# Kernel optimization log

Measured on AMD Instinct MI355X. Metric: run time of the kernel, lower is better.

Reference implementation:

```python
import jax, jax.numpy as jnp
import numpy as np

NEG_SLOPE = 0.2
LN_EPS = 1e-5
NUM_LAYERS = 4
H = 3            # num heads (both modalities)
C_MOL = 512      # molecule channels (in == out, required by the cat in forward)
C_PROT = 1280    # protein channels
VOCAB = 512 * 9 + 1
G_MOL = 512      # molecule graphs
G_PROT = 32      # protein graphs


def _with_self_loops(src, dst, n):
    loop = jnp.arange(n, dtype=src.dtype)
    return jnp.concatenate([src, loop]), jnp.concatenate([dst, loop])


def gat_conv(x, src, dst, W, a_src, a_dst, bias):
    """PyG GATConv, concat=False (head-mean), add_self_loops=True.
    x: [N, Fin], W: [Fin, H*C], a_src/a_dst: [H, C], bias: [C]."""
    n = x.shape[0]
    h = (x @ W).reshape(n, a_src.shape[0], a_src.shape[1])   # [N,H,C]
    al_s = jnp.sum(h * a_src, axis=-1)                       # [N,H]
    al_d = jnp.sum(h * a_dst, axis=-1)                       # [N,H]
    s, d = _with_self_loops(src, dst, n)
    e = jax.nn.leaky_relu(al_s[s] + al_d[d], NEG_SLOPE)      # [E+N,H]
    m = jax.ops.segment_max(e, d, num_segments=n)            # segment softmax (stable)
    m = jnp.where(jnp.isfinite(m), m, 0.0)
    p = jnp.exp(e - m[d])
    z = jax.ops.segment_sum(p, d, num_segments=n)
    alpha = p / (z[d] + 1e-16)                               # [E+N,H]
    out = jax.ops.segment_sum(h[s] * alpha[:, :, None], d, num_segments=n)  # [N,H,C]
    return out.mean(axis=1) + bias                           # concat=False -> head mean


def layer_norm(x, g, b):
    mu = x.mean(-1, keepdims=True)
    var = ((x - mu) ** 2).mean(-1, keepdims=True)
    return (x - mu) * jax.lax.rsqrt(var + LN_EPS) * g + b


def mean_pool(x, batch, num_graphs):
    s = jax.ops.segment_sum(x, batch, num_segments=num_graphs)
    cnt = jax.ops.segment_sum(jnp.ones((x.shape[0],), x.dtype), batch, num_segments=num_graphs)
    return s / jnp.maximum(cnt, 1.0)[:, None]


def setup_inputs() -> dict:
    key = jax.random.key(0)
    ks = jax.random.split(key, 20)
    n_mol, e_mol = 40000, 80000
    n_prot, e_prot = 8000, 64000
    drug_x = jax.random.randint(ks[0], (n_mol, 9), 0, VOCAB)
    mol_edge_index = jax.random.randint(ks[1], (2, e_mol), 0, n_mol)
    mol_batch = jnp.sort(jax.random.randint(ks[2], (n_mol,), 0, G_MOL))
    prot_x = jax.random.normal(ks[3], (n_prot, C_PROT), jnp.float32)
    prot_edge_index = jax.random.randint(ks[4], (2, e_prot), 0, n_prot)
    prot_batch = jnp.sort(jax.random.randint(ks[5], (n_prot,), 0, G_PROT))
    sc = 0.02
    emb = (jax.random.normal(ks[6], (VOCAB, C_MOL), jnp.float32) * sc).at[0].set(0.0)  # padding_idx=0
    mol_W = jax.random.normal(ks[7], (NUM_LAYERS, C_MOL, H * C_MOL), jnp.float32) * sc
    mol_asrc = jax.random.normal(ks[8], (NUM_LAYERS, H, C_MOL), jnp.float32) * sc
    mol_adst = jax.random.normal(ks[9], (NUM_LAYERS, H, C_MOL), jnp.float32) * sc
    mol_bias = jnp.zeros((NUM_LAYERS, C_MOL), jnp.float32)
    mol_ln_g = jnp.ones((NUM_LAYERS, C_MOL), jnp.float32)
    mol_ln_b = jnp.zeros((NUM_LAYERS, C_MOL), jnp.float32)
    prot_W = jax.random.normal(ks[10], (NUM_LAYERS, C_PROT, H * C_PROT), jnp.float32) * sc
    prot_asrc = jax.random.normal(ks[11], (NUM_LAYERS, H, C_PROT), jnp.float32) * sc
    prot_adst = jax.random.normal(ks[12], (NUM_LAYERS, H, C_PROT), jnp.float32) * sc
    prot_bias = jnp.zeros((NUM_LAYERS, C_PROT), jnp.float32)
    prot_ln_g = jnp.ones((NUM_LAYERS, C_PROT), jnp.float32)
    prot_ln_b = jnp.zeros((NUM_LAYERS, C_PROT), jnp.float32)
    return dict(drug_x=drug_x, mol_edge_index=mol_edge_index, mol_batch=mol_batch,
                prot_x=prot_x, prot_edge_index=prot_edge_index, prot_batch=prot_batch,
                emb=emb, mol_W=mol_W, mol_asrc=mol_asrc, mol_adst=mol_adst,
                mol_bias=mol_bias, mol_ln_g=mol_ln_g, mol_ln_b=mol_ln_b,
                prot_W=prot_W, prot_asrc=prot_asrc, prot_adst=prot_adst,
                prot_bias=prot_bias, prot_ln_g=prot_ln_g, prot_ln_b=prot_ln_b)


def reference(drug_x, mol_edge_index, mol_batch, prot_x, prot_edge_index, prot_batch,
              emb, mol_W, mol_asrc, mol_adst, mol_bias, mol_ln_g, mol_ln_b,
              prot_W, prot_asrc, prot_adst, prot_bias, prot_ln_g, prot_ln_b):
    # dropout layers are identity (eval mode)
    mol_x = emb[drug_x].mean(axis=-2)                       # [N_mol, C_MOL]
    mol_feats = [mean_pool(mol_x, mol_batch, G_MOL)]
    prot_feats = [mean_pool(prot_x, prot_batch, G_PROT)]
    msrc, mdst = mol_edge_index[0], mol_edge_index[1]
    psrc, pdst = prot_edge_index[0], prot_edge_index[1]
    px = prot_x
    for i in range(NUM_LAYERS):
        mol_x = gat_conv(mol_x, msrc, mdst, mol_W[i], mol_asrc[i], mol_adst[i], mol_bias[i])
        mol_x = layer_norm(mol_x, mol_ln_g[i], mol_ln_b[i])
        px = gat_conv(px, psrc, pdst, prot_W[i], prot_asrc[i], prot_adst[i], prot_bias[i])
        px = layer_norm(px, prot_ln_g[i], prot_ln_b[i])
        mol_feats.append(mean_pool(mol_x, mol_batch, G_MOL))
        prot_feats.append(mean_pool(px, prot_batch, G_PROT))
    return jnp.stack(mol_feats, axis=1), jnp.stack(prot_feats, axis=1)  # [G,5,C] each
```

## Files before the change

kernel.cpp:

```cpp
#include <hip/hip_runtime.h>
#include <cstdint>


constexpr int H_HEADS = 3;
constexpr float NEG_SLOPE = 0.2f;
constexpr float LN_EPS = 1e-5f;
constexpr int N_MOL = 40000, E_MOL = 80000, C_MOL = 512, G_MOL = 512;
constexpr int N_PROT = 8000, E_PROT = 64000, C_PROT = 1280, G_PROT = 32;
constexpr int LAYERS = 4;
constexpr int MPAD_MOL = 40064;
constexpr int MPAD_PROT = 8064;

typedef unsigned short u16;
typedef __attribute__((ext_vector_type(8))) short short8v;
typedef __attribute__((ext_vector_type(4))) unsigned short ushort4v;
typedef __attribute__((ext_vector_type(4))) float f32x4;

__device__ __forceinline__ float bf2f(u16 s) {
    union { unsigned u; float f; } v; v.u = ((unsigned)s) << 16; return v.f;
}
__device__ __forceinline__ u16 f2bf(float f) {
    union { float f; unsigned u; } v; v.f = f;
    return (u16)((v.u + 0x7fffu + ((v.u >> 16) & 1u)) >> 16);
}

__device__ __forceinline__ void g2l16(const void* g, void* l) {
    __builtin_amdgcn_global_load_lds((const __attribute__((address_space(1))) void*)g,
                                     (__attribute__((address_space(3))) void*)l, 16, 0, 0);
}


__global__ void set_int_kernel(int* p, int v, int n) {
    int i = blockIdx.x * blockDim.x + threadIdx.x;
    if (i < n) p[i] = v;
}

__global__ void zero_f32_kernel(float* p, int n) {
    int i = blockIdx.x * blockDim.x + threadIdx.x;
    if (i < n) p[i] = 0.f;
}

__global__ void copy_int_kernel(const int* __restrict__ s, int* __restrict__ d, int n) {
    int i = blockIdx.x * blockDim.x + threadIdx.x;
    if (i < n) d[i] = s[i];
}

__global__ void hist_kernel(const int* __restrict__ keys, int n, int* __restrict__ cnt) {
    int i = blockIdx.x * blockDim.x + threadIdx.x;
    if (i < n) atomicAdd(&cnt[keys[i]], 1);
}

__global__ void scan_kernel(const int* __restrict__ in, int* __restrict__ out, int n) {
    __shared__ int sums[1024];
    const int t = threadIdx.x;
    const int chunk = (n + 1023) / 1024;
    const int start = t * chunk;
    const int end = min(start + chunk, n);
    int s = 0;
    for (int i = start; i < end; ++i) s += in[i];
    sums[t] = s;
    __syncthreads();
    if (t == 0) {
        int acc = 0;
        for (int i = 0; i < 1024; ++i) { int v = sums[i]; sums[i] = acc; acc += v; }
        out[n] = acc;
    }
    __syncthreads();
    int acc = sums[t];
    for (int i = start; i < end; ++i) { out[i] = acc; acc += in[i]; }
}

__global__ void fill_self_kernel(int* __restrict__ pos, int* __restrict__ srcl, int n) {
    int i = blockIdx.x * blockDim.x + threadIdx.x;
    if (i < n) { int slot = atomicAdd(&pos[i], 1); srcl[slot] = i; }
}

__global__ void fill_edge_kernel(const int* __restrict__ src, const int* __restrict__ dst, int e,
                                 int* __restrict__ pos, int* __restrict__ srcl) {
    int i = blockIdx.x * blockDim.x + threadIdx.x;
    if (i < e) { int slot = atomicAdd(&pos[dst[i]], 1); srcl[slot] = src[i]; }
}

__global__ void f32_to_bf16(const float* __restrict__ in, u16* __restrict__ out, int n) {
    int i = blockIdx.x * blockDim.x + threadIdx.x;
    if (i < n) out[i] = f2bf(in[i]);
}


__global__ void embed_mean_kernel(const int* __restrict__ drug_x, const float* __restrict__ emb,
                                  u16* __restrict__ out) {
    const int n = blockIdx.x;
    __shared__ int idx[9];
    if (threadIdx.x < 9) idx[threadIdx.x] = drug_x[n * 9 + threadIdx.x];
    __syncthreads();
    const int c = threadIdx.x;
    float s = 0.f;
#pragma unroll
    for (int t = 0; t < 9; ++t) s += emb[(size_t)idx[t] * C_MOL + c];
    out[(size_t)n * C_MOL + c] = f2bf(s * (1.f / 9.f));
}


__global__ __launch_bounds__(256) void transfold(const float* __restrict__ W, u16* __restrict__ Wt,
                                                 const float* __restrict__ asrc,
                                                 const float* __restrict__ adst,
                                                 float* __restrict__ wsrc, float* __restrict__ wdst,
                                                 int CIN, int COUT, size_t headStride, int ldn) {
    __shared__ float t[32][33];
    __shared__ float rs[8][33], rd[8][33];
    const int h = blockIdx.z;
    const int n0 = blockIdx.x * 32, k0 = blockIdx.y * 32;
    const int tx = threadIdx.x & 31, ty = threadIdx.x >> 5;
#pragma unroll
    for (int q = 0; q < 4; ++q)
        t[ty + q * 8][tx] = W[(size_t)(k0 + ty + q * 8) * (H_HEADS * COUT) + h * COUT + n0 + tx];
    __syncthreads();
#pragma unroll
    for (int q = 0; q < 4; ++q)
        Wt[(size_t)h * headStride + (size_t)(n0 + ty + q * 8) * ldn + k0 + tx] =
            f2bf(t[tx][ty + q * 8]);
    float ps = 0.f, pd = 0.f;
    const float* as = asrc + h * COUT + n0;
    const float* ad = adst + h * COUT + n0;
#pragma unroll
    for (int q = 0; q < 4; ++q) {
        const float w = t[tx][ty + q * 8];
        ps += w * as[ty + q * 8];
        pd += w * ad[ty + q * 8];
    }
    rs[ty][tx] = ps;
    rd[ty][tx] = pd;
    __syncthreads();
    if (ty == 0) {
        float s = 0.f, d = 0.f;
#pragma unroll
        for (int j = 0; j < 8; ++j) { s += rs[j][tx]; d += rd[j][tx]; }
        atomicAdd(&wsrc[h * CIN + k0 + tx], s);
        atomicAdd(&wdst[h * CIN + k0 + tx], d);
    }
}


template <int C>
__global__ void attn_logits(const u16* __restrict__ x, const float* __restrict__ wsrc,
                            const float* __restrict__ wdst, float* __restrict__ als,
                            float* __restrict__ ald) {
    constexpr int PER = C / 64;
    const int n = blockIdx.x, lane = threadIdx.x;
    const u16* xr = x + (size_t)n * C + lane * PER;
    float xv[PER];
#pragma unroll
    for (int i = 0; i < PER; i += 4) {
        const ushort4v v = *(const ushort4v*)(xr + i);
        xv[i] = bf2f(v.x); xv[i + 1] = bf2f(v.y); xv[i + 2] = bf2f(v.z); xv[i + 3] = bf2f(v.w);
    }
    for (int h = 0; h < H_HEADS; ++h) {
        const float* ws = wsrc + h * C + lane * PER;
        const float* wd = wdst + h * C + lane * PER;
        float ss = 0.f, sd = 0.f;
#pragma unroll
        for (int i = 0; i < PER; i += 4) {
            const float4 a = *(const float4*)(ws + i);
            const float4 b = *(const float4*)(wd + i);
            ss += xv[i] * a.x + xv[i + 1] * a.y + xv[i + 2] * a.z + xv[i + 3] * a.w;
            sd += xv[i] * b.x + xv[i + 1] * b.y + xv[i + 2] * b.z + xv[i + 3] * b.w;
        }
        for (int o = 32; o; o >>= 1) { ss += __shfl_down(ss, o); sd += __shfl_down(sd, o); }
        if (lane == 0) { als[n * H_HEADS + h] = ss; ald[n * H_HEADS + h] = sd; }
    }
}


__global__ void alpha_kernel2(const float* __restrict__ als, const float* __restrict__ ald,
                              const int* __restrict__ indptr, const int* __restrict__ srcl,
                              float* __restrict__ alphaw, int n_nodes) {
    const int t = blockIdx.x * blockDim.x + threadIdx.x;
    const int n = t / H_HEADS, h = t - n * H_HEADS;
    if (n >= n_nodes) return;
    const int beg = indptr[n], end = indptr[n + 1];
    const float ad = ald[n * H_HEADS + h];
    float m = -1e30f;
    for (int e = beg; e < end; ++e) {
        float v = als[srcl[e] * H_HEADS + h] + ad;
        v = v >= 0.f ? v : NEG_SLOPE * v;
        m = fmaxf(m, v);
    }
    float z = 0.f;
    for (int e = beg; e < end; ++e) {
        float v = als[srcl[e] * H_HEADS + h] + ad;
        v = v >= 0.f ? v : NEG_SLOPE * v;
        z += __expf(v - m);
    }
    const float zi = 1.f / (z + 1e-16f);
    for (int e = beg; e < end; ++e) {
        float v = als[srcl[e] * H_HEADS + h] + ad;
        v = v >= 0.f ? v : NEG_SLOPE * v;
        alphaw[e * H_HEADS + h] = __expf(v - m) * zi;
    }
}


__global__ __launch_bounds__(256) void aggregate_mol(const u16* __restrict__ x,
                                                     const float* __restrict__ alphaw,
                                                     const int* __restrict__ indptr,
                                                     const int* __restrict__ srcl,
                                                     u16* __restrict__ agg) {
    const int wv = threadIdx.x >> 6, lane = threadIdx.x & 63;
    const int n = blockIdx.x * 4 + wv;
    const int beg = indptr[n], end = indptr[n + 1];
    float acc[H_HEADS][8];
#pragma unroll
    for (int h = 0; h < H_HEADS; ++h)
#pragma unroll
        for (int j = 0; j < 8; ++j) acc[h][j] = 0.f;
    for (int e = beg; e < end; ++e) {
        const float a0 = alphaw[e * H_HEADS + 0];
        const float a1 = alphaw[e * H_HEADS + 1];
        const float a2 = alphaw[e * H_HEADS + 2];
        const short8v row = *(const short8v*)(x + (size_t)srcl[e] * C_MOL + lane * 8);
#pragma unroll
        for (int j = 0; j < 8; ++j) {
            const float f = bf2f((u16)row[j]);
            acc[0][j] += a0 * f; acc[1][j] += a1 * f; acc[2][j] += a2 * f;
        }
    }
    u16* o = agg + (size_t)n * (3 * C_MOL) + lane * 8;
#pragma unroll
    for (int h = 0; h < H_HEADS; ++h) {
        short8v r;
#pragma unroll
        for (int j = 0; j < 8; ++j) r[j] = (short)f2bf(acc[h][j]);
        *(short8v*)(o + h * C_MOL) = r;
    }
}


template <int C>
__global__ void aggregate_all3(const u16* __restrict__ x, const float* __restrict__ alphaw,
                               const int* __restrict__ indptr, const int* __restrict__ srcl,
                               u16* __restrict__ agg) {
    const int n = blockIdx.x, tid = threadIdx.x;
    const int beg = indptr[n], end = indptr[n + 1];
    float acc[H_HEADS][4];
#pragma unroll
    for (int h = 0; h < H_HEADS; ++h)
#pragma unroll
        for (int j = 0; j < 4; ++j) acc[h][j] = 0.f;
    for (int e = beg; e < end; ++e) {
        const float a0 = alphaw[e * H_HEADS + 0];
        const float a1 = alphaw[e * H_HEADS + 1];
        const float a2 = alphaw[e * H_HEADS + 2];
        const ushort4v v = *(const ushort4v*)(x + (size_t)srcl[e] * C + tid * 4);
        const float f0 = bf2f(v.x), f1 = bf2f(v.y), f2 = bf2f(v.z), f3 = bf2f(v.w);
        acc[0][0] += a0 * f0; acc[0][1] += a0 * f1; acc[0][2] += a0 * f2; acc[0][3] += a0 * f3;
        acc[1][0] += a1 * f0; acc[1][1] += a1 * f1; acc[1][2] += a1 * f2; acc[1][3] += a1 * f3;
        acc[2][0] += a2 * f0; acc[2][1] += a2 * f1; acc[2][2] += a2 * f2; acc[2][3] += a2 * f3;
    }
    u16* o = agg + (size_t)n * (3 * C) + tid * 4;
#pragma unroll
    for (int h = 0; h < H_HEADS; ++h) {
        ushort4v r;
        r.x = f2bf(acc[h][0]); r.y = f2bf(acc[h][1]); r.z = f2bf(acc[h][2]); r.w = f2bf(acc[h][3]);
        *(ushort4v*)(o + h * C) = r;
    }
}


__global__ __launch_bounds__(256) void gemm128d(
    const u16* __restrict__ A0, const u16* __restrict__ B0, u16* __restrict__ C0,
    int N0, int K0, int nx0, int M0, int g0,
    const u16* __restrict__ A1, const u16* __restrict__ B1, u16* __restrict__ C1,
    int N1, int K1, int nx1, int M1) {
    __shared__ u16 lds[16384];
    const int tid = threadIdx.x;
    const int w = tid >> 6, l = tid & 63;
    const int wr = w >> 1, wc = w & 1;

    const int bid = blockIdx.x;
    const u16 *A, *Bt;
    u16* Cout;
    int N, K, nxch, Mreal, base, sz;
    if (bid < g0) { base = 0; sz = g0; A = A0; Bt = B0; Cout = C0; N = N0; K = K0; nxch = nx0; Mreal = M0; }
    else { base = g0; sz = gridDim.x - g0; A = A1; Bt = B1; Cout = C1; N = N1; K = K1; nxch = nx1; Mreal = M1; }
    const int j = bid - base;
    const int q = sz >> 3, r = sz & 7;
    const int xcd = j & 7, idx = j >> 3;
    const int wg = (xcd < r ? xcd * (q + 1) : r * (q + 1) + (xcd - r) * q) + idx;
    const int nx = wg % nxch, my = wg / nxch;
    const size_t bm = (size_t)my * 128, bn = (size_t)nx * 128;

    const f32x4 zf = {0.f, 0.f, 0.f, 0.f};
    f32x4 acc[4][4];
#pragma unroll
    for (int i = 0; i < 4; ++i)
#pragma unroll
        for (int jj = 0; jj < 4; ++jj) acc[i][jj] = zf;

    const int srow = w * 32 + (l >> 3);
    const int sseg = (l & 7) ^ (l >> 3);
    const u16* Ab = A + (bm + srow) * (size_t)K + sseg * 8;
    const u16* Bb = Bt + (bn + srow) * (size_t)K + sseg * 8;

    for (int k0 = 0; k0 < K; k0 += 64) {
#pragma unroll
        for (int qq = 0; qq < 4; ++qq)
            g2l16(Ab + k0 + (size_t)qq * 8 * K, lds + (w * 4 + qq) * 512);
#pragma unroll
        for (int qq = 0; qq < 4; ++qq)
            g2l16(Bb + k0 + (size_t)qq * 8 * K, lds + 8192 + (w * 4 + qq) * 512);
        __syncthreads();
#pragma unroll
        for (int kk = 0; kk < 2; ++kk) {
            const int sg = ((kk * 4 + (l >> 4)) ^ (l & 7)) * 8;
            short8v af[4], bf8[4];
#pragma unroll
            for (int fm = 0; fm < 4; ++fm) {
                const int row = wr * 64 + fm * 16 + (l & 15);
                af[fm] = *(const short8v*)&lds[row * 64 + sg];
            }
#pragma unroll
            for (int fn = 0; fn < 4; ++fn) {
                const int row = wc * 64 + fn * 16 + (l & 15);
                bf8[fn] = *(const short8v*)&lds[8192 + row * 64 + sg];
            }
#pragma unroll
            for (int fm = 0; fm < 4; ++fm)
#pragma unroll
                for (int fn = 0; fn < 4; ++fn)
                    acc[fm][fn] = __builtin_amdgcn_mfma_f32_16x16x32_bf16(af[fm], bf8[fn],
                                                                          acc[fm][fn], 0, 0, 0);
        }
        __syncthreads();
    }

#pragma unroll
    for (int half = 0; half < 2; ++half) {
        if (wr == half) {
#pragma unroll
            for (int fm = 0; fm < 4; ++fm)
#pragma unroll
                for (int fn = 0; fn < 4; ++fn) {
                    const int col = wc * 64 + fn * 16 + (l & 15);
#pragma unroll
                    for (int rr = 0; rr < 4; ++rr)
                        lds[(fm * 16 + (l >> 4) * 4 + rr) * 136 + col] = f2bf(acc[fm][fn][rr]);
                }
        }
        __syncthreads();
        const int lrow = tid >> 2, lseg = tid & 3;
        const size_t grow = bm + half * 64 + lrow;
        if (grow < (size_t)Mreal) {
            u16* Crow = Cout + grow * (size_t)N + bn + lseg * 32;
            const u16* Lr = lds + lrow * 136 + lseg * 32;
#pragma unroll
            for (int ii = 0; ii < 4; ++ii)
                *(float4*)(Crow + ii * 8) = *(const float4*)(Lr + ii * 8);
        }
        __syncthreads();
    }
}


template <int C, int LOGITS>
__global__ __launch_bounds__(256) void ln_kernel(u16* __restrict__ x,
                                                 const float* __restrict__ bias,
                                                 const float* __restrict__ g,
                                                 const float* __restrict__ b,
                                                 const float* __restrict__ wsrc_n,
                                                 const float* __restrict__ wdst_n,
                                                 float* __restrict__ als, float* __restrict__ ald) {
    constexpr int PER = C / 256;
    const int n = blockIdx.x, tid = threadIdx.x;
    u16* xr = x + (size_t)n * C;
    float vals[PER];
    float s1 = 0.f, s2 = 0.f;
    constexpr float invH = 1.f / (float)H_HEADS;
#pragma unroll
    for (int i = 0; i < PER; ++i) {
        const int c = i * 256 + tid;
        const float v = bf2f(xr[c]) * invH + bias[c];
        vals[i] = v;
        s1 += v;
        s2 += v * v;
    }
    __shared__ float red[2][4];
    __shared__ float red2[4][6];
    for (int o = 32; o; o >>= 1) { s1 += __shfl_down(s1, o); s2 += __shfl_down(s2, o); }
    if ((tid & 63) == 0) { red[0][tid >> 6] = s1; red[1][tid >> 6] = s2; }
    __syncthreads();
    const float t1 = red[0][0] + red[0][1] + red[0][2] + red[0][3];
    const float t2 = red[1][0] + red[1][1] + red[1][2] + red[1][3];
    const float mu = t1 / C;
    const float var = t2 / C - mu * mu;
    const float rstd = rsqrtf(var + LN_EPS);
    float ps0 = 0.f, ps1 = 0.f, ps2 = 0.f, pd0 = 0.f, pd1 = 0.f, pd2 = 0.f;
#pragma unroll
    for (int i = 0; i < PER; ++i) {
        const int c = i * 256 + tid;
        const u16 xq16 = f2bf((vals[i] - mu) * rstd * g[c] + b[c]);
        xr[c] = xq16;
        if (LOGITS) {
            const float xq = bf2f(xq16);
            ps0 += xq * wsrc_n[0 * C + c]; pd0 += xq * wdst_n[0 * C + c];
            ps1 += xq * wsrc_n[1 * C + c]; pd1 += xq * wdst_n[1 * C + c];
            ps2 += xq * wsrc_n[2 * C + c]; pd2 += xq * wdst_n[2 * C + c];
        }
    }
    if (LOGITS) {
        for (int o = 32; o; o >>= 1) {
            ps0 += __shfl_down(ps0, o); ps1 += __shfl_down(ps1, o); ps2 += __shfl_down(ps2, o);
            pd0 += __shfl_down(pd0, o); pd1 += __shfl_down(pd1, o); pd2 += __shfl_down(pd2, o);
        }
        __syncthreads();
        if ((tid & 63) == 0) {
            const int wv = tid >> 6;
            red2[wv][0] = ps0; red2[wv][1] = ps1; red2[wv][2] = ps2;
            red2[wv][3] = pd0; red2[wv][4] = pd1; red2[wv][5] = pd2;
        }
        __syncthreads();
        if (tid == 0) {
#pragma unroll
            for (int h = 0; h < H_HEADS; ++h) {
                als[n * H_HEADS + h] = red2[0][h] + red2[1][h] + red2[2][h] + red2[3][h];
                ald[n * H_HEADS + h] =
                    red2[0][3 + h] + red2[1][3 + h] + red2[2][3 + h] + red2[3][3 + h];
            }
        }
    }
}


template <int C, int S>
__global__ void pool_atomic(const u16* __restrict__ x, const int* __restrict__ goff,
                            float* __restrict__ out, int layer) {
    const int g = blockIdx.x, seg = blockIdx.y;
    const int beg = goff[g], end = goff[g + 1];
    const int len = end - beg;
    const int s0 = beg + (len * seg) / S;
    const int s1 = beg + (len * (seg + 1)) / S;
    if (s0 >= s1) return;
    const float inv = 1.f / fmaxf((float)len, 1.f);
    const int tid = threadIdx.x;
    float a0 = 0.f, a1 = 0.f, a2 = 0.f, a3 = 0.f;
    for (int n = s0; n < s1; ++n) {
        const ushort4v v = *(const ushort4v*)(x + (size_t)n * C + tid * 4);
        a0 += bf2f(v.x); a1 += bf2f(v.y); a2 += bf2f(v.z); a3 += bf2f(v.w);
    }
    float* o = out + ((size_t)g * (LAYERS + 1) + layer) * C + tid * 4;
    atomicAdd(o + 0, a0 * inv);
    atomicAdd(o + 1, a1 * inv);
    atomicAdd(o + 2, a2 * inv);
    atomicAdd(o + 3, a3 * inv);
}


extern "C" void kernel_launch(void* const* d_in, const int* in_sizes, int n_in, void* d_out,
                              int out_size, void* d_ws, size_t ws_size, hipStream_t stream) {
    const int* drug_x      = (const int*)d_in[0];
    const int* mol_ei      = (const int*)d_in[1];
    const int* mol_batch   = (const int*)d_in[2];
    const float* prot_in   = (const float*)d_in[3];
    const int* prot_ei     = (const int*)d_in[4];
    const int* prot_batch  = (const int*)d_in[5];
    const float* emb       = (const float*)d_in[6];
    const float* mol_W     = (const float*)d_in[7];
    const float* mol_asrc  = (const float*)d_in[8];
    const float* mol_adst  = (const float*)d_in[9];
    const float* mol_bias  = (const float*)d_in[10];
    const float* mol_lng   = (const float*)d_in[11];
    const float* mol_lnb   = (const float*)d_in[12];
    const float* prot_W    = (const float*)d_in[13];
    const float* prot_asrc = (const float*)d_in[14];
    const float* prot_adst = (const float*)d_in[15];
    const float* prot_bias = (const float*)d_in[16];
    const float* prot_lng  = (const float*)d_in[17];
    const float* prot_lnb  = (const float*)d_in[18];

    if (ws_size < (size_t)240500000) return;
    const bool BIG = ws_size >= (size_t)262000000;

    char* base = (char*)d_ws;
    size_t off = 0;
    auto alloc = [&](size_t bytes) -> void* {
        void* r = base + off;
        off = (off + bytes + 255) & ~(size_t)255;
        return r;
    };
    u16* x_mol  = (u16*)alloc((size_t)N_MOL * C_MOL * 2);
    u16* x_prot = (u16*)alloc((size_t)N_PROT * C_PROT * 2);
    u16* aggM   = (u16*)alloc((size_t)3 * MPAD_MOL * C_MOL * 2);
    u16* WtM    = (u16*)alloc((size_t)H_HEADS * C_MOL * C_MOL * 2);
    u16* WtP    = (u16*)alloc((size_t)H_HEADS * C_PROT * C_PROT * 2);
    u16* aggP   = BIG ? (u16*)alloc((size_t)3 * MPAD_PROT * C_PROT * 2) : aggM;
    float* wsrcM = (float*)alloc((size_t)LAYERS * H_HEADS * C_MOL * 4);
    float* wdstM = (float*)alloc((size_t)LAYERS * H_HEADS * C_MOL * 4);
    float* wsrcP = (float*)alloc((size_t)LAYERS * H_HEADS * C_PROT * 4);
    float* wdstP = (float*)alloc((size_t)LAYERS * H_HEADS * C_PROT * 4);
    float* alsM = (float*)alloc((size_t)N_MOL * H_HEADS * 4);
    float* aldM = (float*)alloc((size_t)N_MOL * H_HEADS * 4);
    float* alsP = (float*)alloc((size_t)N_PROT * H_HEADS * 4);
    float* aldP = (float*)alloc((size_t)N_PROT * H_HEADS * 4);
    float* alphaw = (float*)alloc((size_t)(E_MOL + N_MOL) * H_HEADS * 4);
    int* mol_indptr  = (int*)alloc((N_MOL + 1) * 4);
    int* mol_pos     = (int*)alloc(N_MOL * 4);
    int* mol_srcl    = (int*)alloc((E_MOL + N_MOL) * 4);
    int* prot_indptr = (int*)alloc((N_PROT + 1) * 4);
    int* prot_pos    = (int*)alloc(N_PROT * 4);
    int* prot_srcl   = (int*)alloc((E_PROT + N_PROT) * 4);
    int* cnt         = (int*)alloc(N_MOL * 4);
    int* mol_goff    = (int*)alloc((G_MOL + 1) * 4);
    int* prot_goff   = (int*)alloc((G_PROT + 1) * 4);
    int* gcnt        = (int*)alloc(G_MOL * 4);

    float* out_mol  = (float*)d_out;
    float* out_prot = (float*)d_out + (size_t)G_MOL * (LAYERS + 1) * C_MOL;

    zero_f32_kernel<<<(out_size + 255) / 256, 256, 0, stream>>>((float*)d_out, out_size);
    zero_f32_kernel<<<(LAYERS * H_HEADS * C_MOL + 255) / 256, 256, 0, stream>>>(
        wsrcM, LAYERS * H_HEADS * C_MOL);
    zero_f32_kernel<<<(LAYERS * H_HEADS * C_MOL + 255) / 256, 256, 0, stream>>>(
        wdstM, LAYERS * H_HEADS * C_MOL);
    zero_f32_kernel<<<(LAYERS * H_HEADS * C_PROT + 255) / 256, 256, 0, stream>>>(
        wsrcP, LAYERS * H_HEADS * C_PROT);
    zero_f32_kernel<<<(LAYERS * H_HEADS * C_PROT + 255) / 256, 256, 0, stream>>>(
        wdstP, LAYERS * H_HEADS * C_PROT);

    set_int_kernel<<<(N_MOL + 255) / 256, 256, 0, stream>>>(cnt, 1, N_MOL);
    hist_kernel<<<(E_MOL + 255) / 256, 256, 0, stream>>>(mol_ei + E_MOL, E_MOL, cnt);
    scan_kernel<<<1, 1024, 0, stream>>>(cnt, mol_indptr, N_MOL);
    copy_int_kernel<<<(N_MOL + 255) / 256, 256, 0, stream>>>(mol_indptr, mol_pos, N_MOL);
    fill_self_kernel<<<(N_MOL + 255) / 256, 256, 0, stream>>>(mol_pos, mol_srcl, N_MOL);
    fill_edge_kernel<<<(E_MOL + 255) / 256, 256, 0, stream>>>(mol_ei, mol_ei + E_MOL, E_MOL, mol_pos,
                                                              mol_srcl);
    set_int_kernel<<<(N_PROT + 255) / 256, 256, 0, stream>>>(cnt, 1, N_PROT);
    hist_kernel<<<(E_PROT + 255) / 256, 256, 0, stream>>>(prot_ei + E_PROT, E_PROT, cnt);
    scan_kernel<<<1, 1024, 0, stream>>>(cnt, prot_indptr, N_PROT);
    copy_int_kernel<<<(N_PROT + 255) / 256, 256, 0, stream>>>(prot_indptr, prot_pos, N_PROT);
    fill_self_kernel<<<(N_PROT + 255) / 256, 256, 0, stream>>>(prot_pos, prot_srcl, N_PROT);
    fill_edge_kernel<<<(E_PROT + 255) / 256, 256, 0, stream>>>(prot_ei, prot_ei + E_PROT, E_PROT,
                                                               prot_pos, prot_srcl);

    set_int_kernel<<<(G_MOL + 255) / 256, 256, 0, stream>>>(gcnt, 0, G_MOL);
    hist_kernel<<<(N_MOL + 255) / 256, 256, 0, stream>>>(mol_batch, N_MOL, gcnt);
    scan_kernel<<<1, 1024, 0, stream>>>(gcnt, mol_goff, G_MOL);
    set_int_kernel<<<(G_PROT + 255) / 256, 256, 0, stream>>>(gcnt, 0, G_PROT);
    hist_kernel<<<(N_PROT + 255) / 256, 256, 0, stream>>>(prot_batch, N_PROT, gcnt);
    scan_kernel<<<1, 1024, 0, stream>>>(gcnt, prot_goff, G_PROT);

    transfold<<<dim3(C_MOL / 32, C_MOL / 32, H_HEADS), 256, 0, stream>>>(
        mol_W, WtM, mol_asrc, mol_adst, wsrcM, wdstM, C_MOL, C_MOL, (size_t)C_MOL, 3 * C_MOL);
    transfold<<<dim3(C_PROT / 32, C_PROT / 32, H_HEADS), 256, 0, stream>>>(
        prot_W, WtP, prot_asrc, prot_adst, wsrcP, wdstP, C_PROT, C_PROT, (size_t)C_PROT,
        3 * C_PROT);

    f32_to_bf16<<<(N_PROT * C_PROT + 255) / 256, 256, 0, stream>>>(prot_in, x_prot, N_PROT * C_PROT);
    embed_mean_kernel<<<N_MOL, C_MOL, 0, stream>>>(drug_x, emb, x_mol);
    pool_atomic<C_MOL, 8><<<dim3(G_MOL, 8), C_MOL / 4, 0, stream>>>(x_mol, mol_goff, out_mol, 0);
    pool_atomic<C_PROT, 64><<<dim3(G_PROT, 64), C_PROT / 4, 0, stream>>>(x_prot, prot_goff,
                                                                         out_prot, 0);
    attn_logits<C_MOL><<<N_MOL, 64, 0, stream>>>(x_mol, wsrcM, wdstM, alsM, aldM);
    attn_logits<C_PROT><<<N_PROT, 64, 0, stream>>>(x_prot, wsrcP, wdstP, alsP, aldP);

    const int gMol = (MPAD_MOL / 128) * (C_MOL / 128);
    const int gProt = (MPAD_PROT / 128) * (C_PROT / 128);

    for (int l = 0; l < LAYERS; ++l) {
        const int last = (l == LAYERS - 1);
        if (BIG) {
            alpha_kernel2<<<(N_MOL * H_HEADS + 255) / 256, 256, 0, stream>>>(
                alsM, aldM, mol_indptr, mol_srcl, alphaw, N_MOL);
            aggregate_mol<<<N_MOL / 4, 256, 0, stream>>>(x_mol, alphaw, mol_indptr, mol_srcl, aggM);
            alpha_kernel2<<<(N_PROT * H_HEADS + 255) / 256, 256, 0, stream>>>(
                alsP, aldP, prot_indptr, prot_srcl, alphaw, N_PROT);
            aggregate_all3<C_PROT><<<N_PROT, C_PROT / 4, 0, stream>>>(x_prot, alphaw, prot_indptr,
                                                                      prot_srcl, aggP);
            gemm128d<<<gProt + gMol, 256, 0, stream>>>(
                aggP, WtP, x_prot, C_PROT, 3 * C_PROT, C_PROT / 128, N_PROT, gProt,
                aggM, WtM, x_mol, C_MOL, 3 * C_MOL, C_MOL / 128, N_MOL);
            if (!last) {
                transfold<<<dim3(C_MOL / 32, C_MOL / 32, H_HEADS), 256, 0, stream>>>(
                    mol_W + (size_t)(l + 1) * C_MOL * (H_HEADS * C_MOL), WtM,
                    mol_asrc + (size_t)(l + 1) * H_HEADS * C_MOL,
                    mol_adst + (size_t)(l + 1) * H_HEADS * C_MOL,
                    wsrcM + (size_t)(l + 1) * H_HEADS * C_MOL,
                    wdstM + (size_t)(l + 1) * H_HEADS * C_MOL, C_MOL, C_MOL, (size_t)C_MOL,
                    3 * C_MOL);
                transfold<<<dim3(C_PROT / 32, C_PROT / 32, H_HEADS), 256, 0, stream>>>(
                    prot_W + (size_t)(l + 1) * C_PROT * (H_HEADS * C_PROT), WtP,
                    prot_asrc + (size_t)(l + 1) * H_HEADS * C_PROT,
                    prot_adst + (size_t)(l + 1) * H_HEADS * C_PROT,
                    wsrcP + (size_t)(l + 1) * H_HEADS * C_PROT,
                    wdstP + (size_t)(l + 1) * H_HEADS * C_PROT, C_PROT, C_PROT, (size_t)C_PROT,
                    3 * C_PROT);
                ln_kernel<C_MOL, 1><<<N_MOL, 256, 0, stream>>>(
                    x_mol, mol_bias + (size_t)l * C_MOL, mol_lng + (size_t)l * C_MOL,
                    mol_lnb + (size_t)l * C_MOL, wsrcM + (size_t)(l + 1) * H_HEADS * C_MOL,
                    wdstM + (size_t)(l + 1) * H_HEADS * C_MOL, alsM, aldM);
                ln_kernel<C_PROT, 1><<<N_PROT, 256, 0, stream>>>(
                    x_prot, prot_bias + (size_t)l * C_PROT, prot_lng + (size_t)l * C_PROT,
                    prot_lnb + (size_t)l * C_PROT, wsrcP + (size_t)(l + 1) * H_HEADS * C_PROT,
                    wdstP + (size_t)(l + 1) * H_HEADS * C_PROT, alsP, aldP);
            } else {
                ln_kernel<C_MOL, 0><<<N_MOL, 256, 0, stream>>>(
                    x_mol, mol_bias + (size_t)l * C_MOL, mol_lng + (size_t)l * C_MOL,
                    mol_lnb + (size_t)l * C_MOL, nullptr, nullptr, nullptr, nullptr);
                ln_kernel<C_PROT, 0><<<N_PROT, 256, 0, stream>>>(
                    x_prot, prot_bias + (size_t)l * C_PROT, prot_lng + (size_t)l * C_PROT,
                    prot_lnb + (size_t)l * C_PROT, nullptr, nullptr, nullptr, nullptr);
            }
            pool_atomic<C_MOL, 8><<<dim3(G_MOL, 8), C_MOL / 4, 0, stream>>>(x_mol, mol_goff,
                                                                            out_mol, l + 1);
            pool_atomic<C_PROT, 64><<<dim3(G_PROT, 64), C_PROT / 4, 0, stream>>>(
                x_prot, prot_goff, out_prot, l + 1);
        } else {
            alpha_kernel2<<<(N_MOL * H_HEADS + 255) / 256, 256, 0, stream>>>(
                alsM, aldM, mol_indptr, mol_srcl, alphaw, N_MOL);
            aggregate_mol<<<N_MOL / 4, 256, 0, stream>>>(x_mol, alphaw, mol_indptr, mol_srcl, aggM);
            gemm128d<<<gMol, 256, 0, stream>>>(
                aggM, WtM, x_mol, C_MOL, 3 * C_MOL, C_MOL / 128, N_MOL, gMol,
                aggM, WtM, x_mol, C_MOL, 3 * C_MOL, C_MOL / 128, N_MOL);
            if (!last)
                transfold<<<dim3(C_MOL / 32, C_MOL / 32, H_HEADS), 256, 0, stream>>>(
                    mol_W + (size_t)(l + 1) * C_MOL * (H_HEADS * C_MOL), WtM,
                    mol_asrc + (size_t)(l + 1) * H_HEADS * C_MOL,
                    mol_adst + (size_t)(l + 1) * H_HEADS * C_MOL,
                    wsrcM + (size_t)(l + 1) * H_HEADS * C_MOL,
                    wdstM + (size_t)(l + 1) * H_HEADS * C_MOL, C_MOL, C_MOL, (size_t)C_MOL,
                    3 * C_MOL);
            if (last)
                ln_kernel<C_MOL, 0><<<N_MOL, 256, 0, stream>>>(
                    x_mol, mol_bias + (size_t)l * C_MOL, mol_lng + (size_t)l * C_MOL,
                    mol_lnb + (size_t)l * C_MOL, nullptr, nullptr, nullptr, nullptr);
            else
                ln_kernel<C_MOL, 1><<<N_MOL, 256, 0, stream>>>(
                    x_mol, mol_bias + (size_t)l * C_MOL, mol_lng + (size_t)l * C_MOL,
                    mol_lnb + (size_t)l * C_MOL, wsrcM + (size_t)(l + 1) * H_HEADS * C_MOL,
                    wdstM + (size_t)(l + 1) * H_HEADS * C_MOL, alsM, aldM);
            pool_atomic<C_MOL, 8><<<dim3(G_MOL, 8), C_MOL / 4, 0, stream>>>(x_mol, mol_goff,
                                                                            out_mol, l + 1);
            alpha_kernel2<<<(N_PROT * H_HEADS + 255) / 256, 256, 0, stream>>>(
                alsP, aldP, prot_indptr, prot_srcl, alphaw, N_PROT);
            aggregate_all3<C_PROT><<<N_PROT, C_PROT / 4, 0, stream>>>(x_prot, alphaw, prot_indptr,
                                                                      prot_srcl, aggP);
            gemm128d<<<gProt, 256, 0, stream>>>(
                aggP, WtP, x_prot, C_PROT, 3 * C_PROT, C_PROT / 128, N_PROT, gProt,
                aggP, WtP, x_prot, C_PROT, 3 * C_PROT, C_PROT / 128, N_PROT);
            if (!last)
                transfold<<<dim3(C_PROT / 32, C_PROT / 32, H_HEADS), 256, 0, stream>>>(
                    prot_W + (size_t)(l + 1) * C_PROT * (H_HEADS * C_PROT), WtP,
                    prot_asrc + (size_t)(l + 1) * H_HEADS * C_PROT,
                    prot_adst + (size_t)(l + 1) * H_HEADS * C_PROT,
                    wsrcP + (size_t)(l + 1) * H_HEADS * C_PROT,
                    wdstP + (size_t)(l + 1) * H_HEADS * C_PROT, C_PROT, C_PROT, (size_t)C_PROT,
                    3 * C_PROT);
            if (last)
                ln_kernel<C_PROT, 0><<<N_PROT, 256, 0, stream>>>(
                    x_prot, prot_bias + (size_t)l * C_PROT, prot_lng + (size_t)l * C_PROT,
                    prot_lnb + (size_t)l * C_PROT, nullptr, nullptr, nullptr, nullptr);
            else
                ln_kernel<C_PROT, 1><<<N_PROT, 256, 0, stream>>>(
                    x_prot, prot_bias + (size_t)l * C_PROT, prot_lng + (size_t)l * C_PROT,
                    prot_lnb + (size_t)l * C_PROT, wsrcP + (size_t)(l + 1) * H_HEADS * C_PROT,
                    wdstP + (size_t)(l + 1) * H_HEADS * C_PROT, alsP, aldP);
            pool_atomic<C_PROT, 64><<<dim3(G_PROT, 64), C_PROT / 4, 0, stream>>>(
                x_prot, prot_goff, out_prot, l + 1);
        }
    }
}
```

Baseline: 2.290 ms.

## Fuse attention softmax into aggregation kernels and vectorize layer norm

Removes the separate alpha_kernel2 pass and the alphaw buffer. Each aggregation kernel now computes the per-head segment max and sum for its own node and caches the normalized coefficients in shared memory, falling back to recomputing them when the degree exceeds the table size. This avoids one kernel launch per modality per layer and the global write and read of the edge-weight array, at the cost of a few serial lanes doing the max/sum loops. The layer norm kernel is also reworked to use C/4 threads, each handling four contiguous channels with vector loads, instead of a fixed 256 threads with strided scalar accesses.

```diff
diff --git a/kernel.cpp b/kernel.cpp
--- a/kernel.cpp
+++ b/kernel.cpp
@@ -171,53 +171,70 @@
 }
 
 
-__global__ void alpha_kernel2(const float* __restrict__ als, const float* __restrict__ ald,
-                              const int* __restrict__ indptr, const int* __restrict__ srcl,
-                              float* __restrict__ alphaw, int n_nodes) {
-    const int t = blockIdx.x * blockDim.x + threadIdx.x;
-    const int n = t / H_HEADS, h = t - n * H_HEADS;
-    if (n >= n_nodes) return;
-    const int beg = indptr[n], end = indptr[n + 1];
-    const float ad = ald[n * H_HEADS + h];
-    float m = -1e30f;
-    for (int e = beg; e < end; ++e) {
-        float v = als[srcl[e] * H_HEADS + h] + ad;
-        v = v >= 0.f ? v : NEG_SLOPE * v;
-        m = fmaxf(m, v);
-    }
-    float z = 0.f;
-    for (int e = beg; e < end; ++e) {
-        float v = als[srcl[e] * H_HEADS + h] + ad;
-        v = v >= 0.f ? v : NEG_SLOPE * v;
-        z += __expf(v - m);
-    }
-    const float zi = 1.f / (z + 1e-16f);
-    for (int e = beg; e < end; ++e) {
-        float v = als[srcl[e] * H_HEADS + h] + ad;
-        v = v >= 0.f ? v : NEG_SLOPE * v;
-        alphaw[e * H_HEADS + h] = __expf(v - m) * zi;
-    }
-}
-
-
-__global__ __launch_bounds__(256) void aggregate_mol(const u16* __restrict__ x,
-                                                     const float* __restrict__ alphaw,
-                                                     const int* __restrict__ indptr,
-                                                     const int* __restrict__ srcl,
-                                                     u16* __restrict__ agg) {
+__global__ __launch_bounds__(256) void agg_mol_f(const u16* __restrict__ x,
+                                                 const float* __restrict__ als,
+                                                 const float* __restrict__ ald,
+                                                 const int* __restrict__ indptr,
+                                                 const int* __restrict__ srcl,
+                                                 u16* __restrict__ agg) {
+    constexpr int MAXD = 128;
     const int wv = threadIdx.x >> 6, lane = threadIdx.x & 63;
     const int n = blockIdx.x * 4 + wv;
     const int beg = indptr[n], end = indptr[n + 1];
+    const int deg = end - beg;
+    __shared__ float atab[4][MAXD * 3];
+    float m = -1e30f, zi = 0.f;
+    if (lane < H_HEADS) {
+        const float ad = ald[n * H_HEADS + lane];
+        for (int e = beg; e < end; ++e) {
+            float v = als[srcl[e] * H_HEADS + lane] + ad;
+            v = v >= 0.f ? v : NEG_SLOPE * v;
+            m = fmaxf(m, v);
+        }
+        float z = 0.f;
+        for (int e = beg; e < end; ++e) {
+            float v = als[srcl[e] * H_HEADS + lane] + ad;
+            v = v >= 0.f ? v : NEG_SLOPE * v;
+            z += __expf(v - m);
+        }
+        zi = 1.f / (z + 1e-16f);
+    }
+    const float m0 = __shfl(m, 0), m1 = __shfl(m, 1), m2 = __shfl(m, 2);
+    const float z0 = __shfl(zi, 0), z1 = __shfl(zi, 1), z2 = __shfl(zi, 2);
+    const float ad0 = ald[n * H_HEADS + 0], ad1 = ald[n * H_HEADS + 1], ad2 = ald[n * H_HEADS + 2];
+    const bool fits = deg <= MAXD;
+    if (fits) {
+        for (int i = lane; i < deg * 3; i += 64) {
+            const int e = i / 3, h = i - e * 3;
+            float v = als[srcl[beg + e] * H_HEADS + h] + (h == 0 ? ad0 : (h == 1 ? ad1 : ad2));
+            v = v >= 0.f ? v : NEG_SLOPE * v;
+            const float mh = h == 0 ? m0 : (h == 1 ? m1 : m2);
+            const float zh = h == 0 ? z0 : (h == 1 ? z1 : z2);
+            atab[wv][i] = __expf(v - mh) * zh;
+        }
+    }
+    __syncthreads();
     float acc[H_HEADS][8];
 #pragma unroll
     for (int h = 0; h < H_HEADS; ++h)
 #pragma unroll
         for (int j = 0; j < 8; ++j) acc[h][j] = 0.f;
-    for (int e = beg; e < end; ++e) {
-        const float a0 = alphaw[e * H_HEADS + 0];
-        const float a1 = alphaw[e * H_HEADS + 1];
-        const float a2 = alphaw[e * H_HEADS + 2];
-        const short8v row = *(const short8v*)(x + (size_t)srcl[e] * C_MOL + lane * 8);
+    for (int e = 0; e < deg; ++e) {
+        const int s = srcl[beg + e];
+        float a0, a1, a2;
+        if (fits) {
+            a0 = atab[wv][e * 3 + 0];
+            a1 = atab[wv][e * 3 + 1];
+            a2 = atab[wv][e * 3 + 2];
+        } else {
+            float v0 = als[s * H_HEADS + 0] + ad0; v0 = v0 >= 0.f ? v0 : NEG_SLOPE * v0;
+            float v1 = als[s * H_HEADS + 1] + ad1; v1 = v1 >= 0.f ? v1 : NEG_SLOPE * v1;
+            float v2 = als[s * H_HEADS + 2] + ad2; v2 = v2 >= 0.f ? v2 : NEG_SLOPE * v2;
+            a0 = __expf(v0 - m0) * z0;
+            a1 = __expf(v1 - m1) * z1;
+            a2 = __expf(v2 - m2) * z2;
+        }
+        const short8v row = *(const short8v*)(x + (size_t)s * C_MOL + lane * 8);
 #pragma unroll
         for (int j = 0; j < 8; ++j) {
             const float f = bf2f((u16)row[j]);
@@ -235,33 +252,81 @@
 }
 
 
-template <int C>
-__global__ void aggregate_all3(const u16* __restrict__ x, const float* __restrict__ alphaw,
-                               const int* __restrict__ indptr, const int* __restrict__ srcl,
-                               u16* __restrict__ agg) {
+__global__ __launch_bounds__(320) void agg_prot_f(const u16* __restrict__ x,
+                                                  const float* __restrict__ als,
+                                                  const float* __restrict__ ald,
+                                                  const int* __restrict__ indptr,
+                                                  const int* __restrict__ srcl,
+                                                  u16* __restrict__ agg) {
+    constexpr int MAXD = 512;
     const int n = blockIdx.x, tid = threadIdx.x;
     const int beg = indptr[n], end = indptr[n + 1];
+    const int deg = end - beg;
+    __shared__ float mz[6];
+    __shared__ float atab[MAXD * 3];
+    if (tid < H_HEADS) {
+        const float ad = ald[n * H_HEADS + tid];
+        float m = -1e30f;
+        for (int e = beg; e < end; ++e) {
+            float v = als[srcl[e] * H_HEADS + tid] + ad;
+            v = v >= 0.f ? v : NEG_SLOPE * v;
+            m = fmaxf(m, v);
+        }
+        float z = 0.f;
+        for (int e = beg; e < end; ++e) {
+            float v = als[srcl[e] * H_HEADS + tid] + ad;
+            v = v >= 0.f ? v : NEG_SLOPE * v;
+            z += __expf(v - m);
+        }
+        mz[tid] = m;
+        mz[3 + tid] = 1.f / (z + 1e-16f);
+    }
+    __syncthreads();
+    const bool fits = deg <= MAXD;
+    if (fits) {
+        for (int i = tid; i < deg * 3; i += 320) {
+            const int e = i / 3, h = i - e * 3;
+            float v = als[srcl[beg + e] * H_HEADS + h] + ald[n * H_HEADS + h];
+            v = v >= 0.f ? v : NEG_SLOPE * v;
+            atab[i] = __expf(v - mz[h]) * mz[3 + h];
+        }
+    }
+    __syncthreads();
+    const float m0 = mz[0], m1 = mz[1], m2 = mz[2];
+    const float z0 = mz[3], z1 = mz[4], z2 = mz[5];
+    const float ad0 = ald[n * H_HEADS + 0], ad1 = ald[n * H_HEADS + 1], ad2 = ald[n * H_HEADS + 2];
     float acc[H_HEADS][4];
 #pragma unroll
     for (int h = 0; h < H_HEADS; ++h)
 #pragma unroll
         for (int j = 0; j < 4; ++j) acc[h][j] = 0.f;
-    for (int e = beg; e < end; ++e) {
-        const float a0 = alphaw[e * H_HEADS + 0];
-        const float a1 = alphaw[e * H_HEADS + 1];
-        const float a2 = alphaw[e * H_HEADS + 2];
-        const ushort4v v = *(const ushort4v*)(x + (size_t)srcl[e] * C + tid * 4);
+    for (int e = 0; e < deg; ++e) {
+        const int s = srcl[beg + e];
+        float a0, a1, a2;
+        if (fits) {
+            a0 = atab[e * 3 + 0];
+            a1 = atab[e * 3 + 1];
+            a2 = atab[e * 3 + 2];
+        } else {
+            float v0 = als[s * H_HEADS + 0] + ad0; v0 = v0 >= 0.f ? v0 : NEG_SLOPE * v0;
+            float v1 = als[s * H_HEADS + 1] + ad1; v1 = v1 >= 0.f ? v1 : NEG_SLOPE * v1;
+            float v2 = als[s * H_HEADS + 2] + ad2; v2 = v2 >= 0.f ? v2 : NEG_SLOPE * v2;
+            a0 = __expf(v0 - m0) * z0;
+            a1 = __expf(v1 - m1) * z1;
+            a2 = __expf(v2 - m2) * z2;
+        }
+        const ushort4v v = *(const ushort4v*)(x + (size_t)s * C_PROT + tid * 4);
         const float f0 = bf2f(v.x), f1 = bf2f(v.y), f2 = bf2f(v.z), f3 = bf2f(v.w);
         acc[0][0] += a0 * f0; acc[0][1] += a0 * f1; acc[0][2] += a0 * f2; acc[0][3] += a0 * f3;
         acc[1][0] += a1 * f0; acc[1][1] += a1 * f1; acc[1][2] += a1 * f2; acc[1][3] += a1 * f3;
         acc[2][0] += a2 * f0; acc[2][1] += a2 * f1; acc[2][2] += a2 * f2; acc[2][3] += a2 * f3;
     }
-    u16* o = agg + (size_t)n * (3 * C) + tid * 4;
+    u16* o = agg + (size_t)n * (3 * C_PROT) + tid * 4;
 #pragma unroll
     for (int h = 0; h < H_HEADS; ++h) {
         ushort4v r;
         r.x = f2bf(acc[h][0]); r.y = f2bf(acc[h][1]); r.z = f2bf(acc[h][2]); r.w = f2bf(acc[h][3]);
-        *(ushort4v*)(o + h * C) = r;
+        *(ushort4v*)(o + h * C_PROT) = r;
     }
 }
 
@@ -362,68 +427,77 @@
 
 
 template <int C, int LOGITS>
-__global__ __launch_bounds__(256) void ln_kernel(u16* __restrict__ x,
-                                                 const float* __restrict__ bias,
-                                                 const float* __restrict__ g,
-                                                 const float* __restrict__ b,
-                                                 const float* __restrict__ wsrc_n,
-                                                 const float* __restrict__ wdst_n,
-                                                 float* __restrict__ als, float* __restrict__ ald) {
-    constexpr int PER = C / 256;
+__global__ __launch_bounds__(C / 4) void ln_kernel(u16* __restrict__ x,
+                                                   const float* __restrict__ bias,
+                                                   const float* __restrict__ g,
+                                                   const float* __restrict__ b,
+                                                   const float* __restrict__ wsrc_n,
+                                                   const float* __restrict__ wdst_n,
+                                                   float* __restrict__ als,
+                                                   float* __restrict__ ald) {
+    constexpr int NT = C / 4;
+    constexpr int NW = NT / 64;
     const int n = blockIdx.x, tid = threadIdx.x;
-    u16* xr = x + (size_t)n * C;
-    float vals[PER];
-    float s1 = 0.f, s2 = 0.f;
+    u16* xr = x + (size_t)n * C + tid * 4;
     constexpr float invH = 1.f / (float)H_HEADS;
-#pragma unroll
-    for (int i = 0; i < PER; ++i) {
-        const int c = i * 256 + tid;
-        const float v = bf2f(xr[c]) * invH + bias[c];
-        vals[i] = v;
-        s1 += v;
-        s2 += v * v;
-    }
-    __shared__ float red[2][4];
-    __shared__ float red2[4][6];
+    const ushort4v xv = *(const ushort4v*)xr;
+    const float4 bi = *(const float4*)(bias + tid * 4);
+    const float v0 = bf2f(xv.x) * invH + bi.x;
+    const float v1 = bf2f(xv.y) * invH + bi.y;
+    const float v2 = bf2f(xv.z) * invH + bi.z;
+    const float v3 = bf2f(xv.w) * invH + bi.w;
+    float s1 = v0 + v1 + v2 + v3;
+    float s2 = v0 * v0 + v1 * v1 + v2 * v2 + v3 * v3;
+    __shared__ float red[2][NW];
+    __shared__ float red2[NW][6];
     for (int o = 32; o; o >>= 1) { s1 += __shfl_down(s1, o); s2 += __shfl_down(s2, o); }
     if ((tid & 63) == 0) { red[0][tid >> 6] = s1; red[1][tid >> 6] = s2; }
     __syncthreads();
-    const float t1 = red[0][0] + red[0][1] + red[0][2] + red[0][3];
-    const float t2 = red[1][0] + red[1][1] + red[1][2] + red[1][3];
+    float t1 = 0.f, t2 = 0.f;
+#pragma unroll
+    for (int i = 0; i < NW; ++i) { t1 += red[0][i]; t2 += red[1][i]; }
     const float mu = t1 / C;
     const float var = t2 / C - mu * mu;
     const float rstd = rsqrtf(var + LN_EPS);
-    float ps0 = 0.f, ps1 = 0.f, ps2 = 0.f, pd0 = 0.f, pd1 = 0.f, pd2 = 0.f;
-#pragma unroll
-    for (int i = 0; i < PER; ++i) {
-        const int c = i * 256 + tid;
-        const u16 xq16 = f2bf((vals[i] - mu) * rstd * g[c] + b[c]);
-        xr[c] = xq16;
-        if (LOGITS) {
-            const float xq = bf2f(xq16);
-            ps0 += xq * wsrc_n[0 * C + c]; pd0 += xq * wdst_n[0 * C + c];
-            ps1 += xq * wsrc_n[1 * C + c]; pd1 += xq * wdst_n[1 * C + c];
-            ps2 += xq * wsrc_n[2 * C + c]; pd2 += xq * wdst_n[2 * C + c];
-        }
-    }
+    const float4 gg = *(const float4*)(g + tid * 4);
+    const float4 bb = *(const float4*)(b + tid * 4);
+    ushort4v ov;
+    ov.x = f2bf((v0 - mu) * rstd * gg.x + bb.x);
+    ov.y = f2bf((v1 - mu) * rstd * gg.y + bb.y);
+    ov.z = f2bf((v2 - mu) * rstd * gg.z + bb.z);
+    ov.w = f2bf((v3 - mu) * rstd * gg.w + bb.w);
+    *(ushort4v*)xr = ov;
     if (LOGITS) {
+        const float q0 = bf2f(ov.x), q1 = bf2f(ov.y), q2 = bf2f(ov.z), q3 = bf2f(ov.w);
+        float ps[3], pd[3];
+#pragma unroll
+        for (int h = 0; h < 3; ++h) {
+            const float4 a = *(const float4*)(wsrc_n + h * C + tid * 4);
+            const float4 d = *(const float4*)(wdst_n + h * C + tid * 4);
+            ps[h] = q0 * a.x + q1 * a.y + q2 * a.z + q3 * a.w;
+            pd[h] = q0 * d.x + q1 * d.y + q2 * d.z + q3 * d.w;
+        }
         for (int o = 32; o; o >>= 1) {
-            ps0 += __shfl_down(ps0, o); ps1 += __shfl_down(ps1, o); ps2 += __shfl_down(ps2, o);
-            pd0 += __shfl_down(pd0, o); pd1 += __shfl_down(pd1, o); pd2 += __shfl_down(pd2, o);
-        }
-        __syncthreads();
+#pragma unroll
+            for (int h = 0; h < 3; ++h) {
+                ps[h] += __shfl_down(ps[h], o);
+                pd[h] += __shfl_down(pd[h], o);
+            }
+        }
         if ((tid & 63) == 0) {
             const int wv = tid >> 6;
-            red2[wv][0] = ps0; red2[wv][1] = ps1; red2[wv][2] = ps2;
-            red2[wv][3] = pd0; red2[wv][4] = pd1; red2[wv][5] = pd2;
+#pragma unroll
+            for (int h = 0; h < 3; ++h) { red2[wv][h] = ps[h]; red2[wv][3 + h] = pd[h]; }
         }
         __syncthreads();
         if (tid == 0) {
 #pragma unroll
-            for (int h = 0; h < H_HEADS; ++h) {
-                als[n * H_HEADS + h] = red2[0][h] + red2[1][h] + red2[2][h] + red2[3][h];
-                ald[n * H_HEADS + h] =
-                    red2[0][3 + h] + red2[1][3 + h] + red2[2][3 + h] + red2[3][3 + h];
+            for (int h = 0; h < 3; ++h) {
+                float as = 0.f, ad = 0.f;
+#pragma unroll
+                for (int i = 0; i < NW; ++i) { as += red2[i][h]; ad += red2[i][3 + h]; }
+                als[n * H_HEADS + h] = as;
+                ald[n * H_HEADS + h] = ad;
             }
         }
     }
@@ -500,7 +574,6 @@
     float* aldM = (float*)alloc((size_t)N_MOL * H_HEADS * 4);
     float* alsP = (float*)alloc((size_t)N_PROT * H_HEADS * 4);
     float* aldP = (float*)alloc((size_t)N_PROT * H_HEADS * 4);
-    float* alphaw = (float*)alloc((size_t)(E_MOL + N_MOL) * H_HEADS * 4);
     int* mol_indptr  = (int*)alloc((N_MOL + 1) * 4);
     int* mol_pos     = (int*)alloc(N_MOL * 4);
     int* mol_srcl    = (int*)alloc((E_MOL + N_MOL) * 4);
@@ -567,13 +640,9 @@
     for (int l = 0; l < LAYERS; ++l) {
         const int last = (l == LAYERS - 1);
         if (BIG) {
-            alpha_kernel2<<<(N_MOL * H_HEADS + 255) / 256, 256, 0, stream>>>(
-                alsM, aldM, mol_indptr, mol_srcl, alphaw, N_MOL);
-            aggregate_mol<<<N_MOL / 4, 256, 0, stream>>>(x_mol, alphaw, mol_indptr, mol_srcl, aggM);
-            alpha_kernel2<<<(N_PROT * H_HEADS + 255) / 256, 256, 0, stream>>>(
-                alsP, aldP, prot_indptr, prot_srcl, alphaw, N_PROT);
-            aggregate_all3<C_PROT><<<N_PROT, C_PROT / 4, 0, stream>>>(x_prot, alphaw, prot_indptr,
-                                                                      prot_srcl, aggP);
+            agg_mol_f<<<N_MOL / 4, 256, 0, stream>>>(x_mol, alsM, aldM, mol_indptr, mol_srcl, aggM);
+            agg_prot_f<<<N_PROT, 320, 0, stream>>>(x_prot, alsP, aldP, prot_indptr, prot_srcl,
+                                                   aggP);
             gemm128d<<<gProt + gMol, 256, 0, stream>>>(
                 aggP, WtP, x_prot, C_PROT, 3 * C_PROT, C_PROT / 128, N_PROT, gProt,
                 aggM, WtM, x_mol, C_MOL, 3 * C_MOL, C_MOL / 128, N_MOL);
@@ -592,19 +661,19 @@
                     wsrcP + (size_t)(l + 1) * H_HEADS * C_PROT,
                     wdstP + (size_t)(l + 1) * H_HEADS * C_PROT, C_PROT, C_PROT, (size_t)C_PROT,
                     3 * C_PROT);
-                ln_kernel<C_MOL, 1><<<N_MOL, 256, 0, stream>>>(
+                ln_kernel<C_MOL, 1><<<N_MOL, C_MOL / 4, 0, stream>>>(
                     x_mol, mol_bias + (size_t)l * C_MOL, mol_lng + (size_t)l * C_MOL,
                     mol_lnb + (size_t)l * C_MOL, wsrcM + (size_t)(l + 1) * H_HEADS * C_MOL,
                     wdstM + (size_t)(l + 1) * H_HEADS * C_MOL, alsM, aldM);
-                ln_kernel<C_PROT, 1><<<N_PROT, 256, 0, stream>>>(
+                ln_kernel<C_PROT, 1><<<N_PROT, C_PROT / 4, 0, stream>>>(
                     x_prot, prot_bias + (size_t)l * C_PROT, prot_lng + (size_t)l * C_PROT,
                     prot_lnb + (size_t)l * C_PROT, wsrcP + (size_t)(l + 1) * H_HEADS * C_PROT,
                     wdstP + (size_t)(l + 1) * H_HEADS * C_PROT, alsP, aldP);
             } else {
-                ln_kernel<C_MOL, 0><<<N_MOL, 256, 0, stream>>>(
+                ln_kernel<C_MOL, 0><<<N_MOL, C_MOL / 4, 0, stream>>>(
                     x_mol, mol_bias + (size_t)l * C_MOL, mol_lng + (size_t)l * C_MOL,
                     mol_lnb + (size_t)l * C_MOL, nullptr, nullptr, nullptr, nullptr);
-                ln_kernel<C_PROT, 0><<<N_PROT, 256, 0, stream>>>(
+                ln_kernel<C_PROT, 0><<<N_PROT, C_PROT / 4, 0, stream>>>(
                     x_prot, prot_bias + (size_t)l * C_PROT, prot_lng + (size_t)l * C_PROT,
                     prot_lnb + (size_t)l * C_PROT, nullptr, nullptr, nullptr, nullptr);
             }
@@ -613,9 +682,7 @@
             pool_atomic<C_PROT, 64><<<dim3(G_PROT, 64), C_PROT / 4, 0, stream>>>(
                 x_prot, prot_goff, out_prot, l + 1);
         } else {
-            alpha_kernel2<<<(N_MOL * H_HEADS + 255) / 256, 256, 0, stream>>>(
-                alsM, aldM, mol_indptr, mol_srcl, alphaw, N_MOL);
-            aggregate_mol<<<N_MOL / 4, 256, 0, stream>>>(x_mol, alphaw, mol_indptr, mol_srcl, aggM);
+            agg_mol_f<<<N_MOL / 4, 256, 0, stream>>>(x_mol, alsM, aldM, mol_indptr, mol_srcl, aggM);
             gemm128d<<<gMol, 256, 0, stream>>>(
                 aggM, WtM, x_mol, C_MOL, 3 * C_MOL, C_MOL / 128, N_MOL, gMol,
                 aggM, WtM, x_mol, C_MOL, 3 * C_MOL, C_MOL / 128, N_MOL);
@@ -628,20 +695,18 @@
                     wdstM + (size_t)(l + 1) * H_HEADS * C_MOL, C_MOL, C_MOL, (size_t)C_MOL,
                     3 * C_MOL);
             if (last)
-                ln_kernel<C_MOL, 0><<<N_MOL, 256, 0, stream>>>(
+                ln_kernel<C_MOL, 0><<<N_MOL, C_MOL / 4, 0, stream>>>(
                     x_mol, mol_bias + (size_t)l * C_MOL, mol_lng + (size_t)l * C_MOL,
                     mol_lnb + (size_t)l * C_MOL, nullptr, nullptr, nullptr, nullptr);
             else
-                ln_kernel<C_MOL, 1><<<N_MOL, 256, 0, stream>>>(
+                ln_kernel<C_MOL, 1><<<N_MOL, C_MOL / 4, 0, stream>>>(
                     x_mol, mol_bias + (size_t)l * C_MOL, mol_lng + (size_t)l * C_MOL,
                     mol_lnb + (size_t)l * C_MOL, wsrcM + (size_t)(l + 1) * H_HEADS * C_MOL,
                     wdstM + (size_t)(l + 1) * H_HEADS * C_MOL, alsM, aldM);
             pool_atomic<C_MOL, 8><<<dim3(G_MOL, 8), C_MOL / 4, 0, stream>>>(x_mol, mol_goff,
                                                                             out_mol, l + 1);
-            alpha_kernel2<<<(N_PROT * H_HEADS + 255) / 256, 256, 0, stream>>>(
-                alsP, aldP, prot_indptr, prot_srcl, alphaw, N_PROT);
-            aggregate_all3<C_PROT><<<N_PROT, C_PROT / 4, 0, stream>>>(x_prot, alphaw, prot_indptr,
-                                                                      prot_srcl, aggP);
+            agg_prot_f<<<N_PROT, 320, 0, stream>>>(x_prot, alsP, aldP, prot_indptr, prot_srcl,
+                                                   aggP);
             gemm128d<<<gProt, 256, 0, stream>>>(
                 aggP, WtP, x_prot, C_PROT, 3 * C_PROT, C_PROT / 128, N_PROT, gProt,
                 aggP, WtP, x_prot, C_PROT, 3 * C_PROT, C_PROT / 128, N_PROT);
@@ -654,11 +719,11 @@
                     wdstP + (size_t)(l + 1) * H_HEADS * C_PROT, C_PROT, C_PROT, (size_t)C_PROT,
                     3 * C_PROT);
             if (last)
-                ln_kernel<C_PROT, 0><<<N_PROT, 256, 0, stream>>>(
+                ln_kernel<C_PROT, 0><<<N_PROT, C_PROT / 4, 0, stream>>>(
                     x_prot, prot_bias + (size_t)l * C_PROT, prot_lng + (size_t)l * C_PROT,
                     prot_lnb + (size_t)l * C_PROT, nullptr, nullptr, nullptr, nullptr);
             else
-                ln_kernel<C_PROT, 1><<<N_PROT, 256, 0, stream>>>(
+                ln_kernel<C_PROT, 1><<<N_PROT, C_PROT / 4, 0, stream>>>(
                     x_prot, prot_bias + (size_t)l * C_PROT, prot_lng + (size_t)l * C_PROT,
                     prot_lnb + (size_t)l * C_PROT, wsrcP + (size_t)(l + 1) * H_HEADS * C_PROT,
                     wdstP + (size_t)(l + 1) * H_HEADS * C_PROT, alsP, aldP);
```

Result: no change. 2.271 ms (-0.8%).
